# Performance work log

Hardware: AMD Instinct MI355X
Metric: run time of the kernel (lower is better)

## Reference

```python
import jax, jax.numpy as jnp
import numpy as np

B, C, N = 8, 512, 2048
C4 = C // 4


def setup_inputs() -> dict:
    key = jax.random.key(0)
    ks = jax.random.split(key, 10)
    s = lambda fan: 1.0 / np.sqrt(fan)
    return {
        "x": jax.random.normal(ks[0], (B, C, N), jnp.float32),
        "query": jax.random.normal(ks[1], (B, C, N), jnp.float32),
        "mask": jax.random.randint(ks[2], (B, N), 0, 2, jnp.int32),
        "wqk": jax.random.normal(ks[3], (C4, C), jnp.float32) * s(C),  # shared q/k 1x1 conv
        "wv": jax.random.normal(ks[4], (C, C), jnp.float32) * s(C),
        "bv": jax.random.normal(ks[5], (C,), jnp.float32) * 0.01,
        "wt": jax.random.normal(ks[6], (C, C), jnp.float32) * s(C),
        "bt": jax.random.normal(ks[7], (C,), jnp.float32) * 0.01,
        "gamma": jnp.ones((C,), jnp.float32),
        "beta": jnp.zeros((C,), jnp.float32),
        "rmean": jax.random.normal(ks[8], (C,), jnp.float32) * 0.01,
        "rvar": jax.random.uniform(ks[9], (C,), jnp.float32, 0.5, 1.5),
    }


def reference(x, query, mask, wqk, wv, bv, wt, bt, gamma, beta, rmean, rvar):
    # 1x1 convs == per-point linears (q and k share weights)
    x_q = jnp.einsum("dc,bcn->bnd", wqk, query)            # [B,N,C4]
    x_k = jnp.einsum("dc,bcn->bdn", wqk, x)                # [B,C4,N]
    x_v = jnp.einsum("dc,bcn->bdn", wv, x) + bv[None, :, None]  # [B,C,N]

    energy = jnp.einsum("bnd,bdm->bnm", x_q, x_k)          # [B,N,N]
    m = mask.astype(bool)
    m2 = m[:, :, None] & m[:, None, :]                     # [B,N,N]
    energy = jnp.where(m2, energy, jnp.float32(-9e15))
    d = 1e-9 + m2.sum(axis=1, keepdims=True).astype(energy.dtype)  # [B,1,N]
    attention = jax.nn.softmax(energy / d, axis=-1)

    x_r = jnp.einsum("bcn,bnm->bcm", x_v, attention)       # [B,C,N]
    h = x - x_r
    h = jnp.einsum("dc,bcn->bdn", wt, h) + bt[None, :, None]
    # BatchNorm1d (eval) + ReLU
    inv = gamma / jnp.sqrt(rvar + 1e-5)
    h = (h - rmean[None, :, None]) * inv[None, :, None] + beta[None, :, None]
    h = jax.nn.relu(h)
    return x + h
```

## Files before the change

kernel.cpp:

```cpp
#include <hip/hip_runtime.h>
#include <math.h>

typedef __bf16 bf16;
typedef bf16 bf16x8 __attribute__((ext_vector_type(8)));
typedef bf16 bf16x4 __attribute__((ext_vector_type(4)));
typedef float f32x4 __attribute__((ext_vector_type(4)));

constexpr int kB = 8, kC = 512, kC4 = 128, kN = 2048;

#define MFMA16(a, b, c) __builtin_amdgcn_mfma_f32_16x16x32_bf16(a, b, c, 0, 0, 0)
#define MFMA8(a, b, c) \
  __builtin_amdgcn_mfma_f32_16x16x32_fp8_fp8(a, b, c, 0, 0, 0)

__device__ __forceinline__ unsigned pack4_fp8(float a, float b, float c,
                                              float d) {
  unsigned v = 0;
  v = __builtin_amdgcn_cvt_pk_fp8_f32(a, b, v, false);
  v = __builtin_amdgcn_cvt_pk_fp8_f32(c, d, v, true);
  return v;
}

__global__ __launch_bounds__(256) void k_prep(
    const int* __restrict__ mask, const float* __restrict__ wqk,
    const float* __restrict__ wv, const float* __restrict__ wt,
    const float* __restrict__ gamma, const float* __restrict__ rvar,
    float* __restrict__ cnt, bf16* __restrict__ wqk_bf,
    bf16* __restrict__ wv_bf, bf16* __restrict__ wt_bf,
    float* __restrict__ invg, float* __restrict__ Ssum) {
  const int t = threadIdx.x;
  if (blockIdx.x < 8) {
    const int b = blockIdx.x;
    int s = 0;
    for (int i = t; i < kN; i += 256) s += mask[b * kN + i];
    __shared__ int red[256];
    red[t] = s;
    __syncthreads();
    for (int off = 128; off > 0; off >>= 1) {
      if (t < off) red[t] += red[t + off];
      __syncthreads();
    }
    if (t == 0) cnt[b] = (float)red[0];
    return;
  }
  const int total = 65536 + 262144 + 262144 + 512 + 16384;
  for (int i = (blockIdx.x - 8) * 256 + t; i < total; i += 128 * 256) {
    if (i < 65536) {
      wqk_bf[i] = (bf16)wqk[i];
    } else if (i < 327680) {
      wv_bf[i - 65536] = (bf16)wv[i - 65536];
    } else if (i < 589824) {
      wt_bf[i - 327680] = (bf16)wt[i - 327680];
    } else if (i < 590336) {
      const int j = i - 589824;
      invg[j] = gamma[j] * rsqrtf(rvar[j] + 1e-5f);
    } else {
      Ssum[i - 590336] = 0.0f;
    }
  }
}

__global__ __launch_bounds__(256) void k_tr2(const float* __restrict__ Q,
                                             const float* __restrict__ X,
                                             bf16* __restrict__ XTq,
                                             bf16* __restrict__ XTx) {
  __shared__ float tile[32][69];
  const int z = blockIdx.z, b = z & 7;
  const float* Xs = (z < 8) ? Q : X;
  bf16* XT = (z < 8) ? XTq : XTx;
  const int c0 = blockIdx.y * 32, n0 = blockIdx.x * 64;
  const int t = threadIdx.x;
  const int cc = t >> 4, n4 = (t & 15) * 4;
#pragma unroll
  for (int p = 0; p < 2; p++) {
    const int c = p * 16 + cc;
    const f32x4 v =
        *(const f32x4*)&Xs[((size_t)(b * kC + c0 + c)) * kN + n0 + n4];
    tile[c][n4 + 0] = v[0];
    tile[c][n4 + 1] = v[1];
    tile[c][n4 + 2] = v[2];
    tile[c][n4 + 3] = v[3];
  }
  __syncthreads();
  const int n = t >> 2, c8 = (t & 3) * 8;
  bf16x8 o;
#pragma unroll
  for (int j = 0; j < 8; j++) o[j] = (bf16)tile[c8 + j][n];
  *(bf16x8*)&XT[((size_t)(b * kN + n0 + n)) * kC + c0 + c8] = o;
}

__global__ __launch_bounds__(256, 2) void k_projQK(
    const bf16* __restrict__ XTq, const bf16* __restrict__ XTx,
    const bf16* __restrict__ W, bf16* __restrict__ qT, bf16* __restrict__ kT) {
  __shared__ __align__(16) bf16 As[2][128][32];
  __shared__ __align__(16) bf16 Bs[2][128][32];
  const int nb = blockIdx.x, b = blockIdx.y, src = blockIdx.z;
  const bf16* XT = src ? XTx : XTq;
  bf16* OT = src ? kT : qT;
  const int n0 = nb * 128;
  const int t_ = threadIdx.x, w = t_ >> 6, l = t_ & 63, lo4 = l & 15, g = l >> 4;
  const int mh = w >> 1, ch = w & 1;
  const int srow = w * 16 + (l >> 2), sch = l & 3;
  const int spos = sch ^ ((l >> 3) & 3);
  const int rpos = g ^ ((lo4 >> 1) & 3);
  const bf16* gA0 = &XT[((size_t)(b * kN + n0 + srow)) * kC + sch * 8];
  const bf16* gA1 = gA0 + (size_t)64 * kC;
  const bf16* gB0 = &W[(size_t)srow * kC + sch * 8];
  const bf16* gB1 = gB0 + (size_t)64 * kC;
  f32x4 acc[4][4] = {};
  bf16x8 ra0, ra1, rb0, rb1;
  ra0 = *(const bf16x8*)&gA0[0];
  ra1 = *(const bf16x8*)&gA1[0];
  rb0 = *(const bf16x8*)&gB0[0];
  rb1 = *(const bf16x8*)&gB1[0];
  *(bf16x8*)&As[0][srow][spos * 8] = ra0;
  *(bf16x8*)&As[0][srow + 64][spos * 8] = ra1;
  *(bf16x8*)&Bs[0][srow][spos * 8] = rb0;
  *(bf16x8*)&Bs[0][srow + 64][spos * 8] = rb1;
  __syncthreads();
  for (int tt = 0; tt < 16; tt++) {
    const int buf = tt & 1;
    if (tt < 15) {
      const int k0 = (tt + 1) * 32;
      ra0 = *(const bf16x8*)&gA0[k0];
      ra1 = *(const bf16x8*)&gA1[k0];
      rb0 = *(const bf16x8*)&gB0[k0];
      rb1 = *(const bf16x8*)&gB1[k0];
    }
    bf16x8 af[4], bfr[4];
#pragma unroll
    for (int nf = 0; nf < 4; nf++)
      af[nf] = *(const bf16x8*)&As[buf][mh * 64 + nf * 16 + lo4][rpos * 8];
#pragma unroll
    for (int cf = 0; cf < 4; cf++)
      bfr[cf] = *(const bf16x8*)&Bs[buf][ch * 64 + cf * 16 + lo4][rpos * 8];
#pragma unroll
    for (int nf = 0; nf < 4; nf++)
#pragma unroll
      for (int cf = 0; cf < 4; cf++)
        acc[nf][cf] = MFMA16(af[nf], bfr[cf], acc[nf][cf]);
    if (tt < 15) {
      *(bf16x8*)&As[buf ^ 1][srow][spos * 8] = ra0;
      *(bf16x8*)&As[buf ^ 1][srow + 64][spos * 8] = ra1;
      *(bf16x8*)&Bs[buf ^ 1][srow][spos * 8] = rb0;
      *(bf16x8*)&Bs[buf ^ 1][srow + 64][spos * 8] = rb1;
    }
    __syncthreads();
  }
  bf16* bncw = ((bf16*)As) + w * 16 * 72;
#pragma unroll
  for (int nf = 0; nf < 4; nf++) {
    const int nbase = n0 + mh * 64 + nf * 16;
#pragma unroll
    for (int cf = 0; cf < 4; cf++)
#pragma unroll
      for (int r = 0; r < 4; r++)
        bncw[(4 * g + r) * 72 + cf * 16 + lo4] = (bf16)acc[nf][cf][r];
    const int rr = l >> 2, seg = (l & 3) * 16;
    const bf16x8 v0 = *(const bf16x8*)&bncw[rr * 72 + seg];
    const bf16x8 v1 = *(const bf16x8*)&bncw[rr * 72 + seg + 8];
    bf16* orow = &OT[((size_t)(b * kN + nbase + rr)) * kC4 + ch * 64 + seg];
    *(bf16x8*)&orow[0] = v0;
    *(bf16x8*)&orow[8] = v1;
  }
}

__global__ __launch_bounds__(256, 2) void k_projV(
    const bf16* __restrict__ XTx, const bf16* __restrict__ Wv,
    const float* __restrict__ bv, bf16* __restrict__ xv2) {
  __shared__ __align__(16) bf16 As[2][128][32];
  __shared__ __align__(16) bf16 Bs[2][128][32];
  const int blk = blockIdx.x;
  const int b = blk & 7, tile = blk >> 3;
  const int cb = tile & 3, nb = tile >> 2;
  const int n0 = nb * 128, c0 = cb * 128;
  const int t_ = threadIdx.x, w = t_ >> 6, l = t_ & 63, lo4 = l & 15, g = l >> 4;
  const int mh = w >> 1, ch = w & 1;
  const int srow = w * 16 + (l >> 2), sch = l & 3;
  const int spos = sch ^ ((l >> 3) & 3);
  const int rpos = g ^ ((lo4 >> 1) & 3);
  const bf16* gA0 = &XTx[((size_t)(b * kN + n0 + srow)) * kC + sch * 8];
  const bf16* gA1 = gA0 + (size_t)64 * kC;
  const bf16* gB0 = &Wv[(size_t)(c0 + srow) * kC + sch * 8];
  const bf16* gB1 = gB0 + (size_t)64 * kC;
  f32x4 acc[4][4] = {};
  bf16x8 ra0, ra1, rb0, rb1;
  ra0 = *(const bf16x8*)&gA0[0];
  ra1 = *(const bf16x8*)&gA1[0];
  rb0 = *(const bf16x8*)&gB0[0];
  rb1 = *(const bf16x8*)&gB1[0];
  *(bf16x8*)&As[0][srow][spos * 8] = ra0;
  *(bf16x8*)&As[0][srow + 64][spos * 8] = ra1;
  *(bf16x8*)&Bs[0][srow][spos * 8] = rb0;
  *(bf16x8*)&Bs[0][srow + 64][spos * 8] = rb1;
  __syncthreads();
  for (int tt = 0; tt < 16; tt++) {
    const int buf = tt & 1;
    if (tt < 15) {
      const int k0 = (tt + 1) * 32;
      ra0 = *(const bf16x8*)&gA0[k0];
      ra1 = *(const bf16x8*)&gA1[k0];
      rb0 = *(const bf16x8*)&gB0[k0];
      rb1 = *(const bf16x8*)&gB1[k0];
    }
    bf16x8 af[4], bfr[4];
#pragma unroll
    for (int nf = 0; nf < 4; nf++)
      af[nf] = *(const bf16x8*)&As[buf][mh * 64 + nf * 16 + lo4][rpos * 8];
#pragma unroll
    for (int cf = 0; cf < 4; cf++)
      bfr[cf] = *(const bf16x8*)&Bs[buf][ch * 64 + cf * 16 + lo4][rpos * 8];
#pragma unroll
    for (int nf = 0; nf < 4; nf++)
#pragma unroll
      for (int cf = 0; cf < 4; cf++)
        acc[nf][cf] = MFMA16(af[nf], bfr[cf], acc[nf][cf]);
    if (tt < 15) {
      *(bf16x8*)&As[buf ^ 1][srow][spos * 8] = ra0;
      *(bf16x8*)&As[buf ^ 1][srow + 64][spos * 8] = ra1;
      *(bf16x8*)&Bs[buf ^ 1][srow][spos * 8] = rb0;
      *(bf16x8*)&Bs[buf ^ 1][srow + 64][spos * 8] = rb1;
    }
    __syncthreads();
  }
#pragma unroll
  for (int cf = 0; cf < 4; cf++) {
    const int c = c0 + ch * 64 + cf * 16 + lo4;
    const float bvv = bv[c];
#pragma unroll
    for (int nf = 0; nf < 4; nf++) {
      const int nbase = n0 + mh * 64 + nf * 16 + g * 4;
      bf16x4 o;
#pragma unroll
      for (int r = 0; r < 4; r++) o[r] = (bf16)(acc[nf][cf][r] + bvv);
      *(bf16x4*)&xv2[(((size_t)b * 32 + (nbase >> 6)) * kC + c) * 64 +
                     (nbase & 63)] = o;
    }
  }
}

__global__ __launch_bounds__(256) void k_sum(
    const bf16* __restrict__ qT, const bf16* __restrict__ kT,
    const int* __restrict__ mask, const float* __restrict__ cnt,
    unsigned char* __restrict__ UT8, float* __restrict__ Ssum) {
  __shared__ __align__(16) bf16 kts[2][64][128];
  __shared__ __align__(16) unsigned Ubuf[64][16];
  __shared__ int mss[2][64];
  const int blk = blockIdx.x;
  const int b = blk & 7, nb = (blk >> 3) & 31, mh2 = blk >> 8;
  const int m00 = mh2 * 1024;
  const int t_ = threadIdx.x, w = t_ >> 6, l = t_ & 63, lo4 = l & 15, g = l >> 4;
  const float invd = 1.0f / (cnt[b] + 1e-9f);
  const int n0 = nb * 64;
  bf16x8 aq[4];
#pragma unroll
  for (int ks = 0; ks < 4; ks++)
    aq[ks] = *(const bf16x8*)&qT[((size_t)(b * kN + n0 + w * 16 + lo4)) * kC4 +
                                 ks * 32 + g * 8];
  const int nq = n0 + w * 16 + g * 4;
  const int4 mi = *(const int4*)&mask[b * kN + nq];
  const int mn4[4] = {mi.x, mi.y, mi.z, mi.w};
  float rs4[4] = {0.0f, 0.0f, 0.0f, 0.0f};
  bf16x8 rg[4];
#pragma unroll
  for (int i = 0; i < 4; i++) {
    const int row = w * 16 + i * 4 + g;
    const int q = (l & 15) ^ (row & 7);
    rg[i] = *(const bf16x8*)&kT[((size_t)(b * kN + m00 + row)) * kC4 + q * 8];
  }
#pragma unroll
  for (int i = 0; i < 4; i++) {
    const int row = w * 16 + i * 4 + g;
    *(bf16x8*)&kts[0][row][(l & 15) * 8] = rg[i];
  }
  if (t_ < 16)
    *(int4*)&mss[0][t_ * 4] = *(const int4*)&mask[b * kN + m00 + t_ * 4];
  __syncthreads();
  for (int tt = 0; tt < 16; tt++) {
    const int buf = tt & 1;
    if (tt < 15) {
      const int m0 = m00 + (tt + 1) * 64;
#pragma unroll
      for (int i = 0; i < 4; i++) {
        const int row = w * 16 + i * 4 + g;
        const int q = (l & 15) ^ (row & 7);
        rg[i] = *(const bf16x8*)&kT[((size_t)(b * kN + m0 + row)) * kC4 + q * 8];
      }
    }
#pragma unroll
    for (int mf = 0; mf < 4; mf++) {
      f32x4 e = {};
#pragma unroll
      for (int ks = 0; ks < 4; ks++) {
        const bf16x8 bk =
            *(const bf16x8*)&kts[buf][mf * 16 + lo4]
                                 [((ks * 4 + g) ^ (lo4 & 7)) * 8];
        e = MFMA16(aq[ks], bk, e);
      }
      const int mmv = mss[buf][mf * 16 + lo4];
      float u[4];
#pragma unroll
      for (int r = 0; r < 4; r++) {
        u[r] = mmv ? (mn4[r] ? __expf(e[r] * invd) : 1.0f) : 0.0f;
        rs4[r] += u[r];
      }
      Ubuf[mf * 16 + lo4][(w * 4 + g) ^ lo4] =
          pack4_fp8(u[0], u[1], u[2], u[3]);
    }
    __syncthreads();
    if (tt < 15) {
#pragma unroll
      for (int i = 0; i < 4; i++) {
        const int row = w * 16 + i * 4 + g;
        *(bf16x8*)&kts[buf ^ 1][row][(l & 15) * 8] = rg[i];
      }
      if (t_ < 16)
        *(int4*)&mss[buf ^ 1][t_ * 4] =
            *(const int4*)&mask[b * kN + m00 + (tt + 1) * 64 + t_ * 4];
    }
    {
      const int row = t_ >> 2, q = t_ & 3;
      int4 pkt;
      pkt.x = (int)Ubuf[row][(q * 4 + 0) ^ (row & 15)];
      pkt.y = (int)Ubuf[row][(q * 4 + 1) ^ (row & 15)];
      pkt.z = (int)Ubuf[row][(q * 4 + 2) ^ (row & 15)];
      pkt.w = (int)Ubuf[row][(q * 4 + 3) ^ (row & 15)];
      *(int4*)&UT8[((size_t)(b * kN + m00 + tt * 64 + row)) * kN + n0 +
                   q * 16] = pkt;
    }
    __syncthreads();
  }
#pragma unroll
  for (int r = 0; r < 4; r++) {
#pragma unroll
    for (int off = 1; off < 16; off <<= 1) rs4[r] += __shfl_xor(rs4[r], off);
  }
  if (lo4 == 0) {
#pragma unroll
    for (int r = 0; r < 4; r++) atomicAdd(&Ssum[b * kN + nq + r], rs4[r]);
  }
}

__global__ __launch_bounds__(256) void k_scale(const bf16* __restrict__ xv2,
                                               const float* __restrict__ Ssum,
                                               unsigned* __restrict__ xv8) {
  const int blk = blockIdx.x;
  const int b = blk & 7, part = blk >> 3;
  const size_t base = (size_t)b * (32 * kC * 64);
  for (int it = 0; it < 4; it++) {
    const int chunk = part * 1024 + it * 256 + threadIdx.x;
    const size_t e = (size_t)chunk * 8;
    const int n = ((int)(e >> 15)) * 64 + ((int)e & 63);
    const bf16x8 v = *(const bf16x8*)&xv2[base + e];
    const f32x4 ss0 = *(const f32x4*)&Ssum[b * kN + n];
    const f32x4 ss1 = *(const f32x4*)&Ssum[b * kN + n + 4];
    f32x4 s0, s1;
#pragma unroll
    for (int j = 0; j < 4; j++) {
      s0[j] = 1.0f / ss0[j];
      s1[j] = 1.0f / ss1[j];
    }
    uint2 o;
    o.x = pack4_fp8((float)v[0] * s0[0], (float)v[1] * s0[1],
                    (float)v[2] * s0[2], (float)v[3] * s0[3]);
    o.y = pack4_fp8((float)v[4] * s1[0], (float)v[5] * s1[1],
                    (float)v[6] * s1[2], (float)v[7] * s1[3]);
    *(uint2*)&xv8[(base + e) >> 2] = o;
  }
}

__global__ __launch_bounds__(256, 2) void k_attn2(
    const unsigned char* __restrict__ UT8, const unsigned char* __restrict__ xv8,
    const float* __restrict__ x, bf16* __restrict__ hT) {
  __shared__ __align__(16) unsigned char smem[16384];
  unsigned char (*As)[128][32] = (unsigned char (*)[128][32])smem;
  unsigned char (*Bs)[128][32] = (unsigned char (*)[128][32])(smem + 8192);
  const int blk = blockIdx.x;
  const int b = blk & 7, tile = blk >> 3;
  const int cb = tile & 3, mb = tile >> 2;
  const int m0 = mb * 128, c0 = cb * 128;
  const int t_ = threadIdx.x, w = t_ >> 6, l = t_ & 63, lo4 = l & 15, g = l >> 4;
  const int mh = w >> 1, ch = w & 1;
  const int srow = t_ >> 1, ps = t_ & 1;
  const int m16 = (ps ^ ((srow >> 3) & 1)) * 16;
  const int hsw = (srow >> 2) & 1;
  const int rp8 = (lo4 >> 2) & 3;
  const unsigned char* gA = &UT8[((size_t)(b * kN + m0 + srow)) * kN + ps * 16];
  const unsigned char* gB =
      &xv8[(((size_t)b * 32) * kC + c0 + srow) * 64 + ps * 16];
  f32x4 acc[4][4] = {};
#define STORE_TILE(BUF, VA, VB)                                                \
  {                                                                            \
    int4 sa = VA, sb = VB;                                                     \
    if (hsw) {                                                                 \
      sa.x = (VA).z; sa.y = (VA).w; sa.z = (VA).x; sa.w = (VA).y;              \
      sb.x = (VB).z; sb.y = (VB).w; sb.z = (VB).x; sb.w = (VB).y;              \
    }                                                                          \
    *(int4*)&As[BUF][srow][m16] = sa;                                          \
    *(int4*)&Bs[BUF][srow][m16] = sb;                                          \
  }
  {
    const int4 a = *(const int4*)&gA[0];
    const int4 bb = *(const int4*)&gB[0];
    STORE_TILE(0, a, bb);
  }
  int4 oA, oB, eA, eB;
  oA = *(const int4*)&gA[32];
  oB = *(const int4*)&gB[32];
  __syncthreads();
#define FRAGS_MFMA(BUF)                                                        \
  {                                                                            \
    long af[4], bfr[4];                                                        \
    _Pragma("unroll") for (int mf = 0; mf < 4; mf++) {                         \
      const int row = mh * 64 + mf * 16 + lo4;                                 \
      af[mf] = *(const long*)&As[BUF][row][(g ^ rp8) * 8];                     \
    }                                                                          \
    _Pragma("unroll") for (int cf = 0; cf < 4; cf++) {                         \
      const int row = ch * 64 + cf * 16 + lo4;                                 \
      bfr[cf] = *(const long*)&Bs[BUF][row][(g ^ rp8) * 8];                    \
    }                                                                          \
    _Pragma("unroll") for (int mf = 0; mf < 4; mf++)                           \
        _Pragma("unroll") for (int cf = 0; cf < 4; cf++) acc[mf][cf] =         \
            MFMA8(af[mf], bfr[cf], acc[mf][cf]);                               \
  }
  for (int tt2 = 0; tt2 < 64; tt2 += 2) {
    if (tt2 + 2 < 64) {
      const int n2 = tt2 + 2;
      eA = *(const int4*)&gA[n2 * 32];
      eB = *(const int4*)&gB[(size_t)(n2 >> 1) * (kC * 64) + (n2 & 1) * 32];
    }
    FRAGS_MFMA(0);
    STORE_TILE(1, oA, oB);
    __syncthreads();
    if (tt2 + 3 < 64) {
      const int n3 = tt2 + 3;
      oA = *(const int4*)&gA[n3 * 32];
      oB = *(const int4*)&gB[(size_t)(n3 >> 1) * (kC * 64) + (n3 & 1) * 32];
    }
    FRAGS_MFMA(1);
    if (tt2 + 2 < 64) {
      STORE_TILE(0, eA, eB);
    }
    __syncthreads();
  }
#undef FRAGS_MFMA
#undef STORE_TILE
  bf16* bncw = ((bf16*)smem) + w * 16 * 72;
#pragma unroll
  for (int mf = 0; mf < 4; mf++) {
    const int mbase = m0 + mh * 64 + mf * 16;
    float hh[4][4];
#pragma unroll
    for (int cf = 0; cf < 4; cf++) {
      const int c = c0 + ch * 64 + cf * 16 + lo4;
      const f32x4 xval =
          *(const f32x4*)&x[((size_t)(b * kC + c)) * kN + mbase + g * 4];
#pragma unroll
      for (int r = 0; r < 4; r++) hh[cf][r] = xval[r] - acc[mf][cf][r];
    }
#pragma unroll
    for (int cf = 0; cf < 4; cf++)
#pragma unroll
      for (int r = 0; r < 4; r++)
        bncw[(4 * g + r) * 72 + cf * 16 + lo4] = (bf16)hh[cf][r];
    {
      const int rr = l >> 2, seg = (l & 3) * 16;
      const bf16x8 v0 = *(const bf16x8*)&bncw[rr * 72 + seg];
      const bf16x8 v1 = *(const bf16x8*)&bncw[rr * 72 + seg + 8];
      bf16* orow =
          &hT[((size_t)(b * kN + mbase + rr)) * kC + c0 + ch * 64 + seg];
      *(bf16x8*)&orow[0] = v0;
      *(bf16x8*)&orow[8] = v1;
    }
  }
}

__global__ __launch_bounds__(256, 2) void k_final(
    const bf16* __restrict__ hT, const bf16* __restrict__ wt_bf,
    const float* __restrict__ x, const float* __restrict__ bt,
    const float* __restrict__ beta, const float* __restrict__ rmean,
    const float* __restrict__ invg, float* __restrict__ out) {
  __shared__ __align__(16) bf16 As[2][128][32];
  __shared__ __align__(16) bf16 Bs[2][128][32];
  const int blk = blockIdx.x;
  const int b = blk & 7, tile = blk >> 3;
  const int cb = tile & 3, nb = tile >> 2;
  const int n0 = nb * 128, c0 = cb * 128;
  const int t_ = threadIdx.x, w = t_ >> 6, l = t_ & 63, lo4 = l & 15, g = l >> 4;
  const int mh = w >> 1, ch = w & 1;
  const int srow = w * 16 + (l >> 2), sch = l & 3;
  const int spos = sch ^ ((l >> 3) & 3);
  const int rpos = g ^ ((lo4 >> 1) & 3);
  const bf16* gA0 = &hT[((size_t)(b * kN + n0 + srow)) * kC + sch * 8];
  const bf16* gA1 = gA0 + (size_t)64 * kC;
  const bf16* gB0 = &wt_bf[(size_t)(c0 + srow) * kC + sch * 8];
  const bf16* gB1 = gB0 + (size_t)64 * kC;
  f32x4 acc[4][4] = {};
  bf16x8 ra0, ra1, rb0, rb1;
  ra0 = *(const bf16x8*)&gA0[0];
  ra1 = *(const bf16x8*)&gA1[0];
  rb0 = *(const bf16x8*)&gB0[0];
  rb1 = *(const bf16x8*)&gB1[0];
  *(bf16x8*)&As[0][srow][spos * 8] = ra0;
  *(bf16x8*)&As[0][srow + 64][spos * 8] = ra1;
  *(bf16x8*)&Bs[0][srow][spos * 8] = rb0;
  *(bf16x8*)&Bs[0][srow + 64][spos * 8] = rb1;
  __syncthreads();
  for (int tt = 0; tt < 16; tt++) {
    const int buf = tt & 1;
    if (tt < 15) {
      const int k0 = (tt + 1) * 32;
      ra0 = *(const bf16x8*)&gA0[k0];
      ra1 = *(const bf16x8*)&gA1[k0];
      rb0 = *(const bf16x8*)&gB0[k0];
      rb1 = *(const bf16x8*)&gB1[k0];
    }
    bf16x8 af[4], bfr[4];
#pragma unroll
    for (int nf = 0; nf < 4; nf++)
      af[nf] = *(const bf16x8*)&As[buf][mh * 64 + nf * 16 + lo4][rpos * 8];
#pragma unroll
    for (int cf = 0; cf < 4; cf++)
      bfr[cf] = *(const bf16x8*)&Bs[buf][ch * 64 + cf * 16 + lo4][rpos * 8];
#pragma unroll
    for (int nf = 0; nf < 4; nf++)
#pragma unroll
      for (int cf = 0; cf < 4; cf++)
        acc[nf][cf] = MFMA16(af[nf], bfr[cf], acc[nf][cf]);
    if (tt < 15) {
      *(bf16x8*)&As[buf ^ 1][srow][spos * 8] = ra0;
      *(bf16x8*)&As[buf ^ 1][srow + 64][spos * 8] = ra1;
      *(bf16x8*)&Bs[buf ^ 1][srow][spos * 8] = rb0;
      *(bf16x8*)&Bs[buf ^ 1][srow + 64][spos * 8] = rb1;
    }
    __syncthreads();
  }
#pragma unroll
  for (int cf = 0; cf < 4; cf++) {
    const int c = c0 + ch * 64 + cf * 16 + lo4;
    const float btv = bt[c], rmv = rmean[c], igv = invg[c], bev = beta[c];
#pragma unroll
    for (int nf = 0; nf < 4; nf++) {
      const int nbase = n0 + mh * 64 + nf * 16 + g * 4;
      const size_t base = ((size_t)(b * kC + c)) * kN + nbase;
      const f32x4 xval = *(const f32x4*)&x[base];
      f32x4 o;
#pragma unroll
      for (int r = 0; r < 4; r++) {
        float v = (acc[nf][cf][r] + btv - rmv) * igv + bev;
        v = fmaxf(v, 0.0f);
        o[r] = xval[r] + v;
      }
      *(f32x4*)&out[base] = o;
    }
  }
}

extern "C" void kernel_launch(void* const* d_in, const int* in_sizes, int n_in,
                              void* d_out, int out_size, void* d_ws,
                              size_t ws_size, hipStream_t stream) {
  const float* x = (const float*)d_in[0];
  const float* query = (const float*)d_in[1];
  const int* mask = (const int*)d_in[2];
  const float* wqk = (const float*)d_in[3];
  const float* wv = (const float*)d_in[4];
  const float* bv = (const float*)d_in[5];
  const float* wt = (const float*)d_in[6];
  const float* bt = (const float*)d_in[7];
  const float* gamma = (const float*)d_in[8];
  const float* beta = (const float*)d_in[9];
  const float* rmean = (const float*)d_in[10];
  const float* rvar = (const float*)d_in[11];
  float* out = (float*)d_out;
  char* wsb = (char*)d_ws;

  const size_t MB = 1024 * 1024;
  unsigned char* UT8 = (unsigned char*)wsb;
  bf16* trbufQ = (bf16*)wsb;
  bf16* trbufX = (bf16*)(wsb + 16 * MB);
  bf16* xv2 = (bf16*)(wsb + 32 * MB);
  unsigned* xv8 = (unsigned*)(wsb + 48 * MB);
  bf16* hT = (bf16*)(wsb + 56 * MB);
  bf16* qT = (bf16*)(wsb + 64 * MB);
  bf16* kT = (bf16*)(wsb + 68 * MB);
  bf16* wqk_bf = (bf16*)(wsb + 72 * MB);
  bf16* wv_bf = wqk_bf + 65536;
  bf16* wt_bf = wv_bf + 262144;
  float* invg = (float*)(wt_bf + 262144);
  float* Ssum = invg + 512;
  float* cnt = Ssum + kB * kN;

  k_prep<<<136, 256, 0, stream>>>(mask, wqk, wv, wt, gamma, rvar, cnt, wqk_bf,
                                  wv_bf, wt_bf, invg, Ssum);
  k_tr2<<<dim3(kN / 64, kC / 32, 16), 256, 0, stream>>>(query, x, trbufQ,
                                                        trbufX);
  k_projQK<<<dim3(16, kB, 2), 256, 0, stream>>>(trbufQ, trbufX, wqk_bf, qT,
                                                kT);
  k_projV<<<512, 256, 0, stream>>>(trbufX, wv_bf, bv, xv2);
  k_sum<<<512, 256, 0, stream>>>(qT, kT, mask, cnt, UT8, Ssum);
  k_scale<<<1024, 256, 0, stream>>>(xv2, Ssum, xv8);
  k_attn2<<<512, 256, 0, stream>>>(UT8, (const unsigned char*)xv8, x, hT);
  k_final<<<512, 256, 0, stream>>>(hT, wt_bf, x, bt, beta, rmean, invg, out);
}
```

Baseline: 152.0 us.

## Enlarge attn2 K-tile to 128 fp8 with XOR-swizzled LDS layout

The fp8 attention-times-value GEMM kernel now stages 128-byte K tiles instead of 32-byte ones, so the main loop runs 16 iterations instead of 64. It issues four 16-byte global loads per operand per stage and uses a new 8-byte-granularity XOR swizzle keyed on row to avoid LDS bank conflicts. The aim is to cut the number of __syncthreads barriers and amortise loop overhead over more MFMAs per stage. In exchange, LDS grows from 16KB to 64KB per block and register pressure rises from the extra prefetch buffers, which may hurt the occupancy of two blocks per CU.

```diff
diff --git a/kernel.cpp b/kernel.cpp
--- a/kernel.cpp
+++ b/kernel.cpp
@@ -5,6 +5,7 @@
 typedef bf16 bf16x8 __attribute__((ext_vector_type(8)));
 typedef bf16 bf16x4 __attribute__((ext_vector_type(4)));
 typedef float f32x4 __attribute__((ext_vector_type(4)));
+typedef unsigned long long u64;
 
 constexpr int kB = 8, kC = 512, kC4 = 128, kN = 2048;
 
@@ -369,82 +370,74 @@
 }
 
 __global__ __launch_bounds__(256, 2) void k_attn2(
-    const unsigned char* __restrict__ UT8, const unsigned char* __restrict__ xv8,
-    const float* __restrict__ x, bf16* __restrict__ hT) {
-  __shared__ __align__(16) unsigned char smem[16384];
-  unsigned char (*As)[128][32] = (unsigned char (*)[128][32])smem;
-  unsigned char (*Bs)[128][32] = (unsigned char (*)[128][32])(smem + 8192);
+    const unsigned char* __restrict__ UT8,
+    const unsigned char* __restrict__ xv8, const float* __restrict__ x,
+    bf16* __restrict__ hT) {
+  __shared__ __align__(16) unsigned char As[2][128][128];
+  __shared__ __align__(16) unsigned char Bs[2][128][128];
   const int blk = blockIdx.x;
   const int b = blk & 7, tile = blk >> 3;
   const int cb = tile & 3, mb = tile >> 2;
   const int m0 = mb * 128, c0 = cb * 128;
   const int t_ = threadIdx.x, w = t_ >> 6, l = t_ & 63, lo4 = l & 15, g = l >> 4;
   const int mh = w >> 1, ch = w & 1;
-  const int srow = t_ >> 1, ps = t_ & 1;
-  const int m16 = (ps ^ ((srow >> 3) & 1)) * 16;
-  const int hsw = (srow >> 2) & 1;
-  const int rp8 = (lo4 >> 2) & 3;
-  const unsigned char* gA = &UT8[((size_t)(b * kN + m0 + srow)) * kN + ps * 16];
+  const int srow = t_ >> 1, psl = t_ & 1;
+  const int swk = srow & 15;
+  const unsigned char* gA = &UT8[((size_t)(b * kN + m0 + srow)) * kN + psl * 64];
   const unsigned char* gB =
-      &xv8[(((size_t)b * 32) * kC + c0 + srow) * 64 + ps * 16];
+      &xv8[(((size_t)b * 32 + psl) * kC + c0 + srow) * 64];
   f32x4 acc[4][4] = {};
-#define STORE_TILE(BUF, VA, VB)                                                \
+  ulonglong2 eA[4], eB[4], oA[4], oB[4];
+#define LOADSET(RA, RB, T)                                                     \
   {                                                                            \
-    int4 sa = VA, sb = VB;                                                     \
-    if (hsw) {                                                                 \
-      sa.x = (VA).z; sa.y = (VA).w; sa.z = (VA).x; sa.w = (VA).y;              \
-      sb.x = (VB).z; sb.y = (VB).w; sb.z = (VB).x; sb.w = (VB).y;              \
+    _Pragma("unroll") for (int q = 0; q < 4; q++) {                            \
+      RA[q] = *(const ulonglong2*)&gA[(size_t)(T)*128 + q * 16];               \
+      RB[q] = *(const ulonglong2*)&gB[(size_t)(T)*65536 + q * 16];             \
     }                                                                          \
-    *(int4*)&As[BUF][srow][m16] = sa;                                          \
-    *(int4*)&Bs[BUF][srow][m16] = sb;                                          \
-  }
-  {
-    const int4 a = *(const int4*)&gA[0];
-    const int4 bb = *(const int4*)&gB[0];
-    STORE_TILE(0, a, bb);
-  }
-  int4 oA, oB, eA, eB;
-  oA = *(const int4*)&gA[32];
-  oB = *(const int4*)&gB[32];
-  __syncthreads();
+  }
+#define STORE_TILE(BUF, RA, RB)                                                \
+  {                                                                            \
+    _Pragma("unroll") for (int j = 0; j < 8; j++) {                            \
+      const int v = (psl * 8 + j) ^ swk;                                       \
+      const u64 va = (j & 1) ? RA[j >> 1].y : RA[j >> 1].x;                    \
+      const u64 vb = (j & 1) ? RB[j >> 1].y : RB[j >> 1].x;                    \
+      *(u64*)&As[BUF][srow][v * 8] = va;                                       \
+      *(u64*)&Bs[BUF][srow][v * 8] = vb;                                       \
+    }                                                                          \
+  }
 #define FRAGS_MFMA(BUF)                                                        \
   {                                                                            \
-    long af[4], bfr[4];                                                        \
-    _Pragma("unroll") for (int mf = 0; mf < 4; mf++) {                         \
-      const int row = mh * 64 + mf * 16 + lo4;                                 \
-      af[mf] = *(const long*)&As[BUF][row][(g ^ rp8) * 8];                     \
+    _Pragma("unroll") for (int ks = 0; ks < 4; ks++) {                         \
+      long af[4], bfr[4];                                                      \
+      _Pragma("unroll") for (int mf = 0; mf < 4; mf++) af[mf] =                \
+          *(const long*)&As[BUF][mh * 64 + mf * 16 + lo4]                      \
+                            [((ks * 4 + g) ^ lo4) * 8];                        \
+      _Pragma("unroll") for (int cf = 0; cf < 4; cf++) bfr[cf] =               \
+          *(const long*)&Bs[BUF][ch * 64 + cf * 16 + lo4]                      \
+                            [((ks * 4 + g) ^ lo4) * 8];                        \
+      _Pragma("unroll") for (int mf = 0; mf < 4; mf++)                         \
+          _Pragma("unroll") for (int cf = 0; cf < 4; cf++) acc[mf][cf] =       \
+              MFMA8(af[mf], bfr[cf], acc[mf][cf]);                             \
     }                                                                          \
-    _Pragma("unroll") for (int cf = 0; cf < 4; cf++) {                         \
-      const int row = ch * 64 + cf * 16 + lo4;                                 \
-      bfr[cf] = *(const long*)&Bs[BUF][row][(g ^ rp8) * 8];                    \
-    }                                                                          \
-    _Pragma("unroll") for (int mf = 0; mf < 4; mf++)                           \
-        _Pragma("unroll") for (int cf = 0; cf < 4; cf++) acc[mf][cf] =         \
-            MFMA8(af[mf], bfr[cf], acc[mf][cf]);                               \
-  }
-  for (int tt2 = 0; tt2 < 64; tt2 += 2) {
-    if (tt2 + 2 < 64) {
-      const int n2 = tt2 + 2;
-      eA = *(const int4*)&gA[n2 * 32];
-      eB = *(const int4*)&gB[(size_t)(n2 >> 1) * (kC * 64) + (n2 & 1) * 32];
-    }
+  }
+  LOADSET(eA, eB, 0);
+  STORE_TILE(0, eA, eB);
+  LOADSET(oA, oB, 1);
+  __syncthreads();
+  for (int tt2 = 0; tt2 < 16; tt2 += 2) {
+    if (tt2 + 2 < 16) LOADSET(eA, eB, tt2 + 2);
     FRAGS_MFMA(0);
     STORE_TILE(1, oA, oB);
     __syncthreads();
-    if (tt2 + 3 < 64) {
-      const int n3 = tt2 + 3;
-      oA = *(const int4*)&gA[n3 * 32];
-      oB = *(const int4*)&gB[(size_t)(n3 >> 1) * (kC * 64) + (n3 & 1) * 32];
-    }
+    if (tt2 + 3 < 16) LOADSET(oA, oB, tt2 + 3);
     FRAGS_MFMA(1);
-    if (tt2 + 2 < 64) {
-      STORE_TILE(0, eA, eB);
-    }
+    if (tt2 + 2 < 16) STORE_TILE(0, eA, eB);
     __syncthreads();
   }
 #undef FRAGS_MFMA
 #undef STORE_TILE
-  bf16* bncw = ((bf16*)smem) + w * 16 * 72;
+#undef LOADSET
+  bf16* bncw = ((bf16*)As) + w * 16 * 72;
 #pragma unroll
   for (int mf = 0; mf < 4; mf++) {
     const int mbase = m0 + mh * 64 + mf * 16;
```

After: 147.3 us. 1.03x faster.
